# Kernel tuning notes

Hardware: AMD Instinct MI355X
Metric: run time of the kernel (lower is better)

## Reference

```python
import jax, jax.numpy as jnp
import numpy as np

EPS = 1e-5  # torch BatchNorm1d default eps


def _bn(h, scale, bias):
    # BatchNorm in training mode: biased variance over the node/edge dim.
    mu = h.mean(0)
    var = h.var(0)
    return (h - mu) * jax.lax.rsqrt(var + EPS) * scale + bias


def _segment_mean(msg, idx, n):
    s = jax.ops.segment_sum(msg, idx, num_segments=n)
    cnt = jax.ops.segment_sum(jnp.ones((msg.shape[0],), msg.dtype), idx, num_segments=n)
    return s / jnp.maximum(cnt, 1.0)[:, None]


def setup_inputs() -> dict:
    N, E, D, L = 50000, 800000, 64, 3
    key = jax.random.key(0)
    ks = jax.random.split(key, 7)
    return {
        "x": jax.random.normal(ks[0], (N, D), jnp.float32),
        "edge_attr": jax.random.normal(ks[1], (E, D), jnp.float32),
        "edge_index": jax.random.randint(ks[2], (2, E), 0, N, dtype=jnp.int32),
        "v_w": jax.random.normal(ks[3], (L, 4, D, D), jnp.float32) / np.sqrt(D),
        "v_b": jax.random.normal(ks[4], (L, 4, D), jnp.float32) * 0.02,
        "e_w": jax.random.normal(ks[5], (L, D, D), jnp.float32) / np.sqrt(D),
        "e_b": jax.random.normal(ks[6], (L, D), jnp.float32) * 0.02,
        "vbn_scale": jnp.ones((L, D), jnp.float32),
        "vbn_bias": jnp.zeros((L, D), jnp.float32),
        "ebn_scale": jnp.ones((L, D), jnp.float32),
        "ebn_bias": jnp.zeros((L, D), jnp.float32),
    }


def reference(x, edge_attr, edge_index, v_w, v_b, e_w, e_b,
              vbn_scale, vbn_bias, ebn_scale, ebn_bias):
    n = x.shape[0]
    dst = edge_index[0]  # aggregation target (scatter index)
    src = edge_index[1]  # neighbor node (gather index)
    num_layers = v_w.shape[0]
    w = edge_attr
    for l in range(num_layers):
        x0, w0 = x, w
        # Four node projections in one einsum: [4, N, D]
        xp = jnp.einsum('nd,kde->kne', x0, v_w[l]) + v_b[l][:, None, :]
        x1, x2, x3, x4 = xp[0], xp[1], xp[2], xp[3]
        # Anisotropic edge-gated message passing (vertex update)
        msg = jax.nn.sigmoid(w0) * x2[src]              # [E, D]
        agg = _segment_mean(msg, dst, n)                # [N, D]
        x = x0 + jax.nn.silu(_bn(x1 + agg, vbn_scale[l], vbn_bias[l]))
        # Edge update
        w1 = w0 @ e_w[l] + e_b[l]
        w = w0 + jax.nn.silu(_bn(w1 + x3[dst] + x4[src], ebn_scale[l], ebn_bias[l]))
    return x, w
```

## Files before the change

kernel.cpp:

```cpp
#include <hip/hip_runtime.h>
#include <hip/hip_bf16.h>
#include <math.h>

typedef __attribute__((ext_vector_type(8))) short bf16x8;
typedef __attribute__((ext_vector_type(4))) float f32x4;

__device__ __forceinline__ float bflo(unsigned u) { return __uint_as_float(u << 16); }
__device__ __forceinline__ float bfhi(unsigned u) { return __uint_as_float(u & 0xffff0000u); }
__device__ __forceinline__ unsigned packbf(float a, float b) {
    unsigned ua = __float_as_uint(a), ub = __float_as_uint(b);
    ua += 0x7fffu + ((ua >> 16) & 1u);
    ub += 0x7fffu + ((ub >> 16) & 1u);
    return (ua >> 16) | (ub & 0xffff0000u);
}
__device__ __forceinline__ float silu(float g) { return g / (1.f + __expf(-g)); }

__global__ void zero_int_kernel(int* __restrict__ p, int n) {
    int i = blockIdx.x * blockDim.x + threadIdx.x;
    int s = gridDim.x * blockDim.x;
    for (; i < n; i += s) p[i] = 0;
}

__global__ void count_kernel(const int* __restrict__ dst, int* __restrict__ cnt, int E) {
    int e = blockIdx.x * blockDim.x + threadIdx.x;
    if (e < E) atomicAdd(&cnt[dst[e]], 1);
}

__global__ __launch_bounds__(1024)
void scan_block_kernel(const int* __restrict__ cnt, int* __restrict__ off,
                       int* __restrict__ bsum, int n) {
    __shared__ int wsum[16];
    int tid = threadIdx.x, lane = tid & 63, wid = tid >> 6;
    int i = blockIdx.x * 1024 + tid;
    int v = (i < n) ? cnt[i] : 0;
    int sc = v;
    #pragma unroll
    for (int s = 1; s < 64; s <<= 1) {
        int t = __shfl_up(sc, (unsigned)s, 64);
        if (lane >= s) sc += t;
    }
    if (lane == 63) wsum[wid] = sc;
    __syncthreads();
    int woff = 0;
    for (int k = 0; k < wid; k++) woff += wsum[k];
    if (i < n) off[i + 1] = woff + sc;
    if (tid == 0) {
        int t = 0;
        #pragma unroll
        for (int k = 0; k < 16; k++) t += wsum[k];
        bsum[blockIdx.x] = t;
    }
}

__global__ void scan_tops_kernel(int* __restrict__ bsum, int nb) {
    int lane = threadIdx.x;
    int v = (lane < nb) ? bsum[lane] : 0;
    int sc = v;
    #pragma unroll
    for (int s = 1; s < 64; s <<= 1) {
        int t = __shfl_up(sc, (unsigned)s, 64);
        if (lane >= s) sc += t;
    }
    if (lane < nb) bsum[lane] = sc - v;
}

__global__ __launch_bounds__(1024)
void scan_add_kernel(int* __restrict__ off, const int* __restrict__ bsum, int n) {
    int i = blockIdx.x * 1024 + threadIdx.x;
    int b = bsum[blockIdx.x];
    if (i < n) off[i + 1] += b;
    if (i == 0) off[0] = 0;
}

__global__ void fill_csr_kernel(const int* __restrict__ dst, const int* __restrict__ src,
                                const int* __restrict__ off, int* __restrict__ cnt,
                                int* __restrict__ eidx, int* __restrict__ dstc,
                                int* __restrict__ srcc, int E) {
    int e = blockIdx.x * blockDim.x + threadIdx.x;
    if (e < E) {
        int d = dst[e];
        int pos = atomicSub(&cnt[d], 1) - 1;
        int slot = off[d] + pos;
        eidx[slot] = e;
        dstc[slot] = d;
        srcc[slot] = src[e];
    }
}

__global__ void pack_kernel(const float* __restrict__ v_w, const float* __restrict__ e_w,
                            short* __restrict__ vwp, short* __restrict__ ewp, int L) {
    int t = blockIdx.x * blockDim.x + threadIdx.x;
    if (t >= L * 5 * 4 * 2 * 64) return;
    int lane = t & 63;
    int ks = (t >> 6) & 1;
    int ft = (t >> 7) & 3;
    int mat = t >> 9;
    int layer = mat / 5, mi = mat % 5;
    const float* W = (mi < 4) ? (v_w + (long long)(layer * 4 + mi) * 4096)
                              : (e_w + (long long)layer * 4096);
    int m = ft * 16 + (lane & 15);
    int k0 = ks * 32 + (lane >> 4) * 8;
    short* dstp = (mi < 4)
        ? vwp + ((((long long)(layer * 4 + mi) * 4 + ft) * 2 + ks) * 64 + lane) * 8
        : ewp + ((((long long)layer * 4 + ft) * 2 + ks) * 64 + lane) * 8;
    #pragma unroll
    for (int j = 0; j < 8; j++) {
        unsigned u = __float_as_uint(W[(k0 + j) * 64 + m]);
        u += 0x7fffu + ((u >> 16) & 1u);
        dstp[j] = (short)(u >> 16);
    }
}

__global__ __launch_bounds__(256)
void node_gemm_mfma(const float* __restrict__ X, const short* __restrict__ vwp,
                    const float* __restrict__ vb, __hip_bfloat16* __restrict__ xp,
                    int Nn) {
    __shared__ short Xs[64 * 64];
    __shared__ short Hs[4][64 * 64];
    int tid = threadIdx.x;
    long long row0 = (long long)blockIdx.x * 64;

    {
        int r = tid >> 2, cq = tid & 3;
        long long row = row0 + r;
        float4 v0 = {0,0,0,0}, v1 = {0,0,0,0}, v2 = {0,0,0,0}, v3 = {0,0,0,0};
        if (row < Nn) {
            const float* sp = X + row * 64 + cq * 16;
            v0 = *(const float4*)(sp);     v1 = *(const float4*)(sp + 4);
            v2 = *(const float4*)(sp + 8); v3 = *(const float4*)(sp + 12);
        }
        uint4 w0, w1;
        w0.x = packbf(v0.x, v0.y); w0.y = packbf(v0.z, v0.w);
        w0.z = packbf(v1.x, v1.y); w0.w = packbf(v1.z, v1.w);
        w1.x = packbf(v2.x, v2.y); w1.y = packbf(v2.z, v2.w);
        w1.z = packbf(v3.x, v3.y); w1.w = packbf(v3.z, v3.w);
        int base = r * 128 + cq * 32, swz = (r & 7) << 4;
        *(uint4*)((char*)Xs + (base ^ swz)) = w0;
        *(uint4*)((char*)Xs + ((base + 16) ^ swz)) = w1;
    }
    __syncthreads();

    int l = tid & 63, wv = tid >> 6;
    int rl = wv * 16 + (l & 15);
    bf16x8 bfr[2];
    #pragma unroll
    for (int ks = 0; ks < 2; ks++) {
        int off = (rl * 128 + ks * 64 + (l >> 4) * 16) ^ ((rl & 7) << 4);
        bfr[ks] = *(bf16x8*)((char*)Xs + off);
    }
    int q4 = (l >> 4) * 4;
    for (int g = 0; g < 4; g++) {
        #pragma unroll
        for (int ft = 0; ft < 4; ft++) {
            f32x4 acc = f32x4{0.f, 0.f, 0.f, 0.f};
            #pragma unroll
            for (int ks = 0; ks < 2; ks++) {
                bf16x8 a = *(const bf16x8*)(vwp + (((long long)(g * 4 + ft) * 2 + ks) * 64 + l) * 8);
                acc = __builtin_amdgcn_mfma_f32_16x16x32_bf16(a, bfr[ks], acc, 0, 0, 0);
            }
            int f0 = ft * 16 + q4;
            float4 bv = *(const float4*)&vb[g * 64 + f0];
            uint2 o;
            o.x = packbf(acc[0] + bv.x, acc[1] + bv.y);
            o.y = packbf(acc[2] + bv.z, acc[3] + bv.w);
            int hoff = (rl * 128 + f0 * 2) ^ ((rl & 7) << 4);
            *(uint2*)((char*)Hs[g] + hoff) = o;
        }
    }
    __syncthreads();
    int r = tid >> 2, cc = (tid & 3) * 16;
    long long node = row0 + r;
    if (node < Nn) {
        int swz = (r & 7) << 4;
        #pragma unroll
        for (int g = 0; g < 4; g++) {
            uint4 a = *(uint4*)((char*)Hs[g] + ((r * 128 + cc * 2) ^ swz));
            uint4 b = *(uint4*)((char*)Hs[g] + ((r * 128 + cc * 2 + 16) ^ swz));
            __hip_bfloat16* op = xp + ((long long)g * Nn + node) * 64 + cc;
            *(uint4*)op = a;
            *(uint4*)(op + 8) = b;
        }
    }
}

template <int MODE>
__global__ __launch_bounds__(256)
void edge_gemm_mfma(const float* __restrict__ ea, const int* __restrict__ eidx,
                    __hip_bfloat16* __restrict__ w_csr, __hip_bfloat16* __restrict__ h_e,
                    const float* __restrict__ fin,
                    const short* __restrict__ ewp, const float* __restrict__ eb,
                    const __hip_bfloat16* __restrict__ x3, const __hip_bfloat16* __restrict__ x4,
                    const int* __restrict__ dstc, const int* __restrict__ srcc,
                    float* __restrict__ estats) {
    __shared__ short Ws[64 * 64];
    __shared__ short Hs[64 * 68];
    __shared__ float sredS[4][64], sredQ[4][64];
    __shared__ int dstl[64], srcl[64];
    int tid = threadIdx.x;
    long long row0 = (long long)blockIdx.x * 64;

    {
        int r = tid >> 2, cq = tid & 3;
        long long grow = (row0 + r) * 64 + cq * 16;
        int base = r * 128 + cq * 32, swz = (r & 7) << 4;
        uint4 w0u, w1u;
        if (MODE == 0) {
            long long e0 = eidx[row0 + r];
            const float* sp = ea + e0 * 64 + cq * 16;
            float4 v0 = *(const float4*)(sp),     v1 = *(const float4*)(sp + 4);
            float4 v2 = *(const float4*)(sp + 8), v3 = *(const float4*)(sp + 12);
            w0u.x = packbf(v0.x, v0.y); w0u.y = packbf(v0.z, v0.w);
            w0u.z = packbf(v1.x, v1.y); w0u.w = packbf(v1.z, v1.w);
            w1u.x = packbf(v2.x, v2.y); w1u.y = packbf(v2.z, v2.w);
            w1u.z = packbf(v3.x, v3.y); w1u.w = packbf(v3.z, v3.w);
        } else {
            uint4 a = *(const uint4*)&w_csr[grow];
            uint4 b = *(const uint4*)&w_csr[grow + 8];
            unsigned ua[8] = {a.x, a.y, a.z, a.w, b.x, b.y, b.z, b.w};
            uint4 ha = *(const uint4*)&h_e[grow];
            uint4 hb = *(const uint4*)&h_e[grow + 8];
            unsigned uh[8] = {ha.x, ha.y, ha.z, ha.w, hb.x, hb.y, hb.z, hb.w};
            const float* kmp = fin + 128 + cq * 16;
            const float* kap = fin + 192 + cq * 16;
            float wn[16];
            #pragma unroll
            for (int j = 0; j < 8; j++) {
                wn[2*j]   = bflo(ua[j]) + silu(bflo(uh[j]) * kmp[2*j]   + kap[2*j]);
                wn[2*j+1] = bfhi(ua[j]) + silu(bfhi(uh[j]) * kmp[2*j+1] + kap[2*j+1]);
            }
            w0u.x = packbf(wn[0], wn[1]);  w0u.y = packbf(wn[2], wn[3]);
            w0u.z = packbf(wn[4], wn[5]);  w0u.w = packbf(wn[6], wn[7]);
            w1u.x = packbf(wn[8], wn[9]);  w1u.y = packbf(wn[10], wn[11]);
            w1u.z = packbf(wn[12], wn[13]); w1u.w = packbf(wn[14], wn[15]);
        }
        *(uint4*)&w_csr[grow] = w0u;
        *(uint4*)&w_csr[grow + 8] = w1u;
        *(uint4*)((char*)Ws + (base ^ swz)) = w0u;
        *(uint4*)((char*)Ws + ((base + 16) ^ swz)) = w1u;
        if (tid < 64) {
            dstl[tid] = dstc[row0 + tid];
            srcl[tid] = srcc[row0 + tid];
        }
    }
    __syncthreads();

    int rr0 = tid >> 3, rr1 = rr0 + 32;
    int c8 = (tid & 7) * 8;
    int de0 = dstl[rr0], se0 = srcl[rr0];
    int de1 = dstl[rr1], se1 = srcl[rr1];
    uint4 g3a = *(const uint4*)&x3[(long long)de0 * 64 + c8];
    uint4 g4a = *(const uint4*)&x4[(long long)se0 * 64 + c8];
    uint4 g3b = *(const uint4*)&x3[(long long)de1 * 64 + c8];
    uint4 g4b = *(const uint4*)&x4[(long long)se1 * 64 + c8];

    int l = tid & 63, wv = tid >> 6;
    int rl = wv * 16 + (l & 15);
    bf16x8 bfr[2];
    #pragma unroll
    for (int ks = 0; ks < 2; ks++) {
        int off = (rl * 128 + ks * 64 + (l >> 4) * 16) ^ ((rl & 7) << 4);
        bfr[ks] = *(bf16x8*)((char*)Ws + off);
    }
    int q4 = (l >> 4) * 4;
    #pragma unroll
    for (int ft = 0; ft < 4; ft++) {
        f32x4 acc = f32x4{0.f, 0.f, 0.f, 0.f};
        #pragma unroll
        for (int ks = 0; ks < 2; ks++) {
            bf16x8 a = *(const bf16x8*)(ewp + (((long long)ft * 2 + ks) * 64 + l) * 8);
            acc = __builtin_amdgcn_mfma_f32_16x16x32_bf16(a, bfr[ks], acc, 0, 0, 0);
        }
        int f0 = ft * 16 + q4;
        float4 bv = *(const float4*)&eb[f0];
        uint2 o;
        o.x = packbf(acc[0] + bv.x, acc[1] + bv.y);
        o.y = packbf(acc[2] + bv.z, acc[3] + bv.w);
        *(uint2*)&Hs[rl * 68 + f0] = o;
    }
    __syncthreads();

    float s[8], q[8];
    #pragma unroll
    for (int j = 0; j < 8; j++) { s[j] = 0.f; q[j] = 0.f; }
    #pragma unroll
    for (int p = 0; p < 2; p++) {
        int rr = p ? rr1 : rr0;
        uint4 g3 = p ? g3b : g3a;
        uint4 g4 = p ? g4b : g4a;
        unsigned u3[4] = {g3.x, g3.y, g3.z, g3.w};
        unsigned u4[4] = {g4.x, g4.y, g4.z, g4.w};
        uint4 hu = *(uint4*)&Hs[rr * 68 + c8];
        unsigned uh[4] = {hu.x, hu.y, hu.z, hu.w};
        float h[8];
        #pragma unroll
        for (int j = 0; j < 4; j++) {
            float h0 = bflo(uh[j]) + bflo(u3[j]) + bflo(u4[j]);
            float h1 = bfhi(uh[j]) + bfhi(u3[j]) + bfhi(u4[j]);
            h[2*j] = h0; h[2*j+1] = h1;
            s[2*j] += h0; s[2*j+1] += h1;
            q[2*j] += h0 * h0; q[2*j+1] += h1 * h1;
        }
        uint4 hv;
        hv.x = packbf(h[0], h[1]); hv.y = packbf(h[2], h[3]);
        hv.z = packbf(h[4], h[5]); hv.w = packbf(h[6], h[7]);
        *(uint4*)&h_e[(row0 + rr) * 64 + c8] = hv;
    }
    #pragma unroll
    for (int d = 8; d < 64; d <<= 1) {
        #pragma unroll
        for (int j = 0; j < 8; j++) {
            s[j] += __shfl_xor(s[j], d);
            q[j] += __shfl_xor(q[j], d);
        }
    }
    if ((l >> 3) == 0) {
        #pragma unroll
        for (int j = 0; j < 8; j++) {
            sredS[wv][(l & 7) * 8 + j] = s[j];
            sredQ[wv][(l & 7) * 8 + j] = q[j];
        }
    }
    __syncthreads();
    if (tid < 128) {
        int which = tid >> 6, f = tid & 63;
        float v = which ? (sredQ[0][f] + sredQ[1][f] + sredQ[2][f] + sredQ[3][f])
                        : (sredS[0][f] + sredS[1][f] + sredS[2][f] + sredS[3][f]);
        atomicAdd(&estats[(blockIdx.x & 7) * 128 + which * 64 + f], v);
    }
}

template <bool FINAL>
__global__ __launch_bounds__(256)
void node_finish_kernel(const __hip_bfloat16* __restrict__ w_csr, const int* __restrict__ srcc,
                        const __hip_bfloat16* __restrict__ x2, const __hip_bfloat16* __restrict__ x1,
                        const int* __restrict__ off, float* __restrict__ h_v,
                        float* __restrict__ nstats,
                        const __hip_bfloat16* __restrict__ h_e, const int* __restrict__ eidx,
                        float* __restrict__ out_w, const float* __restrict__ fin,
                        int Nn, int E) {
    __shared__ float red[8 * 66];
    __shared__ float km[64], ka[64];
    int tid = threadIdx.x;
    if (FINAL) {
        if (tid < 64) { km[tid] = fin[128 + tid]; ka[tid] = fin[192 + tid]; }
        __syncthreads();
    }
    int hw = tid >> 5, k = tid & 31;
    int n = blockIdx.x * 8 + hw;
    float h0 = 0.f, h1 = 0.f;
    if (n < Nn) {
        int o0 = off[n], o1 = off[n + 1];
        float a0 = 0.f, a1 = 0.f;
        int j = o0;
        for (; j + 1 < o1; j += 2) {
            int s0 = srcc[j], s1 = srcc[j + 1];
            unsigned wu0 = *(const unsigned*)&w_csr[(long long)j * 64 + 2 * k];
            unsigned wu1 = *(const unsigned*)&w_csr[(long long)(j + 1) * 64 + 2 * k];
            unsigned xu0 = *(const unsigned*)&x2[(long long)s0 * 64 + 2 * k];
            unsigned xu1 = *(const unsigned*)&x2[(long long)s1 * 64 + 2 * k];
            a0 += bflo(xu0) / (1.f + __expf(-bflo(wu0)))
                + bflo(xu1) / (1.f + __expf(-bflo(wu1)));
            a1 += bfhi(xu0) / (1.f + __expf(-bfhi(wu0)))
                + bfhi(xu1) / (1.f + __expf(-bfhi(wu1)));
        }
        if (j < o1) {
            int s0 = srcc[j];
            unsigned wu0 = *(const unsigned*)&w_csr[(long long)j * 64 + 2 * k];
            unsigned xu0 = *(const unsigned*)&x2[(long long)s0 * 64 + 2 * k];
            a0 += bflo(xu0) / (1.f + __expf(-bflo(wu0)));
            a1 += bfhi(xu0) / (1.f + __expf(-bfhi(wu0)));
        }
        float ic = 1.f / fmaxf((float)(o1 - o0), 1.f);
        unsigned xu = *(const unsigned*)&x1[(long long)n * 64 + 2 * k];
        h0 = bflo(xu) + a0 * ic;
        h1 = bfhi(xu) + a1 * ic;
        *(float2*)&h_v[(long long)n * 64 + 2 * k] = make_float2(h0, h1);
    }
    red[hw * 66 + 2 * k] = h0;
    red[hw * 66 + 2 * k + 1] = h1;
    __syncthreads();
    float* nst = nstats + (blockIdx.x & 7) * 128;
    if (tid < 64) {
        float s = 0.f;
        #pragma unroll
        for (int r = 0; r < 8; r++) s += red[r * 66 + tid];
        atomicAdd(&nst[tid], s);
    }
    __syncthreads();
    red[hw * 66 + 2 * k] = h0 * h0;
    red[hw * 66 + 2 * k + 1] = h1 * h1;
    __syncthreads();
    if (tid < 64) {
        float s = 0.f;
        #pragma unroll
        for (int r = 0; r < 8; r++) s += red[r * 66 + tid];
        atomicAdd(&nst[64 + tid], s);
    }
    if (FINAL) {
        long long total = (long long)E * 32;
        for (long long u = (long long)blockIdx.x * 256 + tid; u < total;
             u += (long long)gridDim.x * 256) {
            long long row = u >> 5;
            int kk = (int)(u & 31);
            unsigned wu = *(const unsigned*)&w_csr[row * 64 + 2 * kk];
            unsigned hu = *(const unsigned*)&h_e[row * 64 + 2 * kk];
            int e = eidx[row];
            float o0 = bflo(wu) + silu(bflo(hu) * km[2 * kk]     + ka[2 * kk]);
            float o1 = bfhi(wu) + silu(bfhi(hu) * km[2 * kk + 1] + ka[2 * kk + 1]);
            *(float2*)&out_w[(long long)e * 64 + 2 * kk] = make_float2(o0, o1);
        }
    }
}

__global__ void finalize_edge_kernel(const float* __restrict__ estats,
                                     const float* __restrict__ es, const float* __restrict__ eb,
                                     float* __restrict__ fin, float invE) {
    int c = threadIdx.x;
    float s = 0.f, q = 0.f;
    #pragma unroll
    for (int r = 0; r < 8; r++) { s += estats[r * 128 + c]; q += estats[r * 128 + 64 + c]; }
    float mean = s * invE;
    float var = q * invE - mean * mean;
    float kmul = rsqrtf(var + 1e-5f) * es[c];
    fin[128 + c] = kmul;
    fin[192 + c] = eb[c] - mean * kmul;
}

__global__ void finalize_node_kernel(const float* __restrict__ nstats,
                                     const float* __restrict__ vs, const float* __restrict__ vb,
                                     float* __restrict__ fin, float invN) {
    int c = threadIdx.x;
    float s = 0.f, q = 0.f;
    #pragma unroll
    for (int r = 0; r < 8; r++) { s += nstats[r * 128 + c]; q += nstats[r * 128 + 64 + c]; }
    float mean = s * invN;
    float var = q * invN - mean * mean;
    float kmul = rsqrtf(var + 1e-5f) * vs[c];
    fin[c] = kmul;
    fin[64 + c] = vb[c] - mean * kmul;
}

__global__ __launch_bounds__(256)
void node_apply_kernel(const float4* __restrict__ hv4, const float4* __restrict__ xold4,
                       float4* __restrict__ out4, const float* __restrict__ fin, int total) {
    __shared__ float km[64], ka[64];
    if (threadIdx.x < 64) { km[threadIdx.x] = fin[threadIdx.x]; ka[threadIdx.x] = fin[64 + threadIdx.x]; }
    __syncthreads();
    int idx = blockIdx.x * 256 + threadIdx.x;
    if (idx >= total) return;
    int c0 = (idx & 15) * 4;
    float4 h = hv4[idx], xo = xold4[idx];
    float4 m = *(float4*)&km[c0], a = *(float4*)&ka[c0];
    float g0 = h.x * m.x + a.x, g1 = h.y * m.y + a.y, g2 = h.z * m.z + a.z, g3 = h.w * m.w + a.w;
    out4[idx] = make_float4(xo.x + silu(g0), xo.y + silu(g1),
                            xo.z + silu(g2), xo.w + silu(g3));
}

extern "C" void kernel_launch(void* const* d_in, const int* in_sizes, int n_in,
                              void* d_out, int out_size, void* d_ws, size_t ws_size,
                              hipStream_t stream) {
    const float* x_in  = (const float*)d_in[0];
    const float* ea_in = (const float*)d_in[1];
    const int*   ei    = (const int*)d_in[2];
    const float* v_w   = (const float*)d_in[3];
    const float* v_b   = (const float*)d_in[4];
    const float* e_w   = (const float*)d_in[5];
    const float* e_b   = (const float*)d_in[6];
    const float* vbn_s = (const float*)d_in[7];
    const float* vbn_b = (const float*)d_in[8];
    const float* ebn_s = (const float*)d_in[9];
    const float* ebn_b = (const float*)d_in[10];

    const int Nn = in_sizes[0] / 64;
    const int E  = in_sizes[1] / 64;
    const int L  = in_sizes[3] / (4 * 64 * 64);

    const int* dst = ei;
    const int* src = ei + E;

    float* h_v    = (float*)d_ws;
    float* nstats = h_v + (long long)Nn * 64;
    float* estats = nstats + (long long)L * 1024;
    float* fin    = estats + (long long)L * 1024;
    __hip_bfloat16* xp    = (__hip_bfloat16*)(fin + 256);
    __hip_bfloat16* h_e   = xp + (long long)4 * Nn * 64;
    __hip_bfloat16* w_csr = h_e + (long long)E * 64;
    short* vwp = (short*)(w_csr + (long long)E * 64);
    short* ewp = vwp + (long long)L * 16384;
    int* cnt  = (int*)(ewp + (long long)L * 4096);
    int* off  = cnt + Nn;
    int* eidx = off + Nn + 1;
    int* dstc = eidx + E;
    int* srcc = dstc + E;
    int* bsum = srcc + E;

    size_t needed = ((size_t)Nn * 64 + (size_t)L * 2048 + 256) * 4 +
                    ((size_t)4 * Nn * 64 + (size_t)2 * E * 64 + (size_t)L * 20480) * 2 +
                    ((size_t)2 * Nn + 1 + (size_t)3 * E + 64) * 4;
    if (ws_size < needed) return;

    float* out_x = (float*)d_out;
    float* out_w = out_x + (long long)Nn * 64;

    const int nb = (Nn + 1023) / 1024;
    zero_int_kernel<<<64, 256, 0, stream>>>(cnt, Nn);
    zero_int_kernel<<<8, 256, 0, stream>>>((int*)nstats, L * 2048);
    count_kernel<<<(E + 255) / 256, 256, 0, stream>>>(dst, cnt, E);
    scan_block_kernel<<<nb, 1024, 0, stream>>>(cnt, off, bsum, Nn);
    scan_tops_kernel<<<1, 64, 0, stream>>>(bsum, nb);
    scan_add_kernel<<<nb, 1024, 0, stream>>>(off, bsum, Nn);
    fill_csr_kernel<<<(E + 255) / 256, 256, 0, stream>>>(dst, src, off, cnt, eidx, dstc, srcc, E);
    pack_kernel<<<(L * 2560 + 255) / 256, 256, 0, stream>>>(v_w, e_w, vwp, ewp, L);

    const __hip_bfloat16* x1 = xp;
    const __hip_bfloat16* x2 = xp + (long long)Nn * 64;
    const __hip_bfloat16* x3 = xp + (long long)2 * Nn * 64;
    const __hip_bfloat16* x4 = xp + (long long)3 * Nn * 64;

    for (int l = 0; l < L; l++) {
        const float* xl = (l == 0) ? x_in : out_x;
        bool last = (l == L - 1);
        float* nst = nstats + (long long)l * 1024;
        float* est = estats + (long long)l * 1024;

        node_gemm_mfma<<<(Nn + 63) / 64, 256, 0, stream>>>(
            xl, vwp + (long long)l * 16384, v_b + l * 256, xp, Nn);

        if (l == 0)
            edge_gemm_mfma<0><<<E / 64, 256, 0, stream>>>(
                ea_in, eidx, w_csr, h_e, fin, ewp + (long long)l * 4096, e_b + l * 64,
                x3, x4, dstc, srcc, est);
        else
            edge_gemm_mfma<1><<<E / 64, 256, 0, stream>>>(
                ea_in, eidx, w_csr, h_e, fin, ewp + (long long)l * 4096, e_b + l * 64,
                x3, x4, dstc, srcc, est);

        finalize_edge_kernel<<<1, 64, 0, stream>>>(
            est, ebn_s + l * 64, ebn_b + l * 64, fin, 1.f / (float)E);

        if (last)
            node_finish_kernel<true><<<(Nn + 7) / 8, 256, 0, stream>>>(
                w_csr, srcc, x2, x1, off, h_v, nst, h_e, eidx, out_w, fin, Nn, E);
        else
            node_finish_kernel<false><<<(Nn + 7) / 8, 256, 0, stream>>>(
                w_csr, srcc, x2, x1, off, h_v, nst, h_e, eidx, out_w, fin, Nn, E);

        finalize_node_kernel<<<1, 64, 0, stream>>>(
            nst, vbn_s + l * 64, vbn_b + l * 64, fin, 1.f / (float)Nn);

        node_apply_kernel<<<(Nn * 16 + 255) / 256, 256, 0, stream>>>(
            (const float4*)h_v, (const float4*)xl, (float4*)out_x, fin, Nn * 16);
    }
}
```

Before: 718.0 us.

## Recompute previous-layer edge pre-activation instead of storing h_e; fuse final edge output

Intermediate layers no longer write the bf16 edge pre-activation h_e. The next layer's edge kernel instead recomputes it from the previous layer's weights and double-buffered x3/x4 projections, then applies the BN/SiLU residual update in shared memory. The final edge output write moves into the node_finish CSR loop rather than running as a separate grid-stride pass. This trades E*64 bf16 of store plus reload traffic per layer for an extra small MFMA GEMM and extra gathers, and it doubles the node projection buffer.

```diff
diff --git a/kernel.cpp b/kernel.cpp
--- a/kernel.cpp
+++ b/kernel.cpp
@@ -183,12 +183,14 @@
     }
 }
 
-template <int MODE>
+template <bool FIRST, bool LAST>
 __global__ __launch_bounds__(256)
 void edge_gemm_mfma(const float* __restrict__ ea, const int* __restrict__ eidx,
                     __hip_bfloat16* __restrict__ w_csr, __hip_bfloat16* __restrict__ h_e,
                     const float* __restrict__ fin,
+                    const short* __restrict__ ewp_p, const float* __restrict__ eb_p,
                     const short* __restrict__ ewp, const float* __restrict__ eb,
+                    const __hip_bfloat16* __restrict__ x3p, const __hip_bfloat16* __restrict__ x4p,
                     const __hip_bfloat16* __restrict__ x3, const __hip_bfloat16* __restrict__ x4,
                     const int* __restrict__ dstc, const int* __restrict__ srcc,
                     float* __restrict__ estats) {
@@ -204,7 +206,7 @@
         long long grow = (row0 + r) * 64 + cq * 16;
         int base = r * 128 + cq * 32, swz = (r & 7) << 4;
         uint4 w0u, w1u;
-        if (MODE == 0) {
+        if (FIRST) {
             long long e0 = eidx[row0 + r];
             const float* sp = ea + e0 * 64 + cq * 16;
             float4 v0 = *(const float4*)(sp),     v1 = *(const float4*)(sp + 4);
@@ -213,28 +215,12 @@
             w0u.z = packbf(v1.x, v1.y); w0u.w = packbf(v1.z, v1.w);
             w1u.x = packbf(v2.x, v2.y); w1u.y = packbf(v2.z, v2.w);
             w1u.z = packbf(v3.x, v3.y); w1u.w = packbf(v3.z, v3.w);
+            *(uint4*)&w_csr[grow] = w0u;
+            *(uint4*)&w_csr[grow + 8] = w1u;
         } else {
-            uint4 a = *(const uint4*)&w_csr[grow];
-            uint4 b = *(const uint4*)&w_csr[grow + 8];
-            unsigned ua[8] = {a.x, a.y, a.z, a.w, b.x, b.y, b.z, b.w};
-            uint4 ha = *(const uint4*)&h_e[grow];
-            uint4 hb = *(const uint4*)&h_e[grow + 8];
-            unsigned uh[8] = {ha.x, ha.y, ha.z, ha.w, hb.x, hb.y, hb.z, hb.w};
-            const float* kmp = fin + 128 + cq * 16;
-            const float* kap = fin + 192 + cq * 16;
-            float wn[16];
-            #pragma unroll
-            for (int j = 0; j < 8; j++) {
-                wn[2*j]   = bflo(ua[j]) + silu(bflo(uh[j]) * kmp[2*j]   + kap[2*j]);
-                wn[2*j+1] = bfhi(ua[j]) + silu(bfhi(uh[j]) * kmp[2*j+1] + kap[2*j+1]);
-            }
-            w0u.x = packbf(wn[0], wn[1]);  w0u.y = packbf(wn[2], wn[3]);
-            w0u.z = packbf(wn[4], wn[5]);  w0u.w = packbf(wn[6], wn[7]);
-            w1u.x = packbf(wn[8], wn[9]);  w1u.y = packbf(wn[10], wn[11]);
-            w1u.z = packbf(wn[12], wn[13]); w1u.w = packbf(wn[14], wn[15]);
-        }
-        *(uint4*)&w_csr[grow] = w0u;
-        *(uint4*)&w_csr[grow + 8] = w1u;
+            w0u = *(const uint4*)&w_csr[grow];
+            w1u = *(const uint4*)&w_csr[grow + 8];
+        }
         *(uint4*)((char*)Ws + (base ^ swz)) = w0u;
         *(uint4*)((char*)Ws + ((base + 16) ^ swz)) = w1u;
         if (tid < 64) {
@@ -244,24 +230,86 @@
     }
     __syncthreads();
 
+    int l = tid & 63, wv = tid >> 6;
+    int rl = wv * 16 + (l & 15);
+    int q4 = (l >> 4) * 4;
     int rr0 = tid >> 3, rr1 = rr0 + 32;
     int c8 = (tid & 7) * 8;
     int de0 = dstl[rr0], se0 = srcl[rr0];
     int de1 = dstl[rr1], se1 = srcl[rr1];
+
+    if (!FIRST) {
+        uint4 p3a = *(const uint4*)&x3p[(long long)de0 * 64 + c8];
+        uint4 p4a = *(const uint4*)&x4p[(long long)se0 * 64 + c8];
+        uint4 p3b = *(const uint4*)&x3p[(long long)de1 * 64 + c8];
+        uint4 p4b = *(const uint4*)&x4p[(long long)se1 * 64 + c8];
+
+        bf16x8 bfr[2];
+        #pragma unroll
+        for (int ks = 0; ks < 2; ks++) {
+            int off = (rl * 128 + ks * 64 + (l >> 4) * 16) ^ ((rl & 7) << 4);
+            bfr[ks] = *(bf16x8*)((char*)Ws + off);
+        }
+        #pragma unroll
+        for (int ft = 0; ft < 4; ft++) {
+            f32x4 acc = f32x4{0.f, 0.f, 0.f, 0.f};
+            #pragma unroll
+            for (int ks = 0; ks < 2; ks++) {
+                bf16x8 a = *(const bf16x8*)(ewp_p + (((long long)ft * 2 + ks) * 64 + l) * 8);
+                acc = __builtin_amdgcn_mfma_f32_16x16x32_bf16(a, bfr[ks], acc, 0, 0, 0);
+            }
+            int f0 = ft * 16 + q4;
+            float4 bv = *(const float4*)&eb_p[f0];
+            uint2 o;
+            o.x = packbf(acc[0] + bv.x, acc[1] + bv.y);
+            o.y = packbf(acc[2] + bv.z, acc[3] + bv.w);
+            *(uint2*)&Hs[rl * 68 + f0] = o;
+        }
+        __syncthreads();
+
+        float4 km0 = *(const float4*)&fin[128 + c8], km1 = *(const float4*)&fin[128 + c8 + 4];
+        float4 ka0 = *(const float4*)&fin[192 + c8], ka1 = *(const float4*)&fin[192 + c8 + 4];
+        float kmv[8] = {km0.x, km0.y, km0.z, km0.w, km1.x, km1.y, km1.z, km1.w};
+        float kav[8] = {ka0.x, ka0.y, ka0.z, ka0.w, ka1.x, ka1.y, ka1.z, ka1.w};
+        #pragma unroll
+        for (int p = 0; p < 2; p++) {
+            int rr = p ? rr1 : rr0;
+            uint4 p3 = p ? p3b : p3a;
+            uint4 p4 = p ? p4b : p4a;
+            unsigned u3[4] = {p3.x, p3.y, p3.z, p3.w};
+            unsigned u4[4] = {p4.x, p4.y, p4.z, p4.w};
+            uint4 hu = *(uint4*)&Hs[rr * 68 + c8];
+            unsigned uh[4] = {hu.x, hu.y, hu.z, hu.w};
+            int woff = (rr * 128 + c8 * 2) ^ ((rr & 7) << 4);
+            uint4 wu = *(uint4*)((char*)Ws + woff);
+            unsigned uw[4] = {wu.x, wu.y, wu.z, wu.w};
+            float wn[8];
+            #pragma unroll
+            for (int j = 0; j < 4; j++) {
+                float h0 = bflo(uh[j]) + bflo(u3[j]) + bflo(u4[j]);
+                float h1 = bfhi(uh[j]) + bfhi(u3[j]) + bfhi(u4[j]);
+                wn[2*j]   = bflo(uw[j]) + silu(h0 * kmv[2*j]   + kav[2*j]);
+                wn[2*j+1] = bfhi(uw[j]) + silu(h1 * kmv[2*j+1] + kav[2*j+1]);
+            }
+            uint4 wo;
+            wo.x = packbf(wn[0], wn[1]); wo.y = packbf(wn[2], wn[3]);
+            wo.z = packbf(wn[4], wn[5]); wo.w = packbf(wn[6], wn[7]);
+            *(uint4*)((char*)Ws + woff) = wo;
+            *(uint4*)&w_csr[(row0 + rr) * 64 + c8] = wo;
+        }
+        __syncthreads();
+    }
+
     uint4 g3a = *(const uint4*)&x3[(long long)de0 * 64 + c8];
     uint4 g4a = *(const uint4*)&x4[(long long)se0 * 64 + c8];
     uint4 g3b = *(const uint4*)&x3[(long long)de1 * 64 + c8];
     uint4 g4b = *(const uint4*)&x4[(long long)se1 * 64 + c8];
-
-    int l = tid & 63, wv = tid >> 6;
-    int rl = wv * 16 + (l & 15);
     bf16x8 bfr[2];
     #pragma unroll
     for (int ks = 0; ks < 2; ks++) {
         int off = (rl * 128 + ks * 64 + (l >> 4) * 16) ^ ((rl & 7) << 4);
         bfr[ks] = *(bf16x8*)((char*)Ws + off);
     }
-    int q4 = (l >> 4) * 4;
     #pragma unroll
     for (int ft = 0; ft < 4; ft++) {
         f32x4 acc = f32x4{0.f, 0.f, 0.f, 0.f};
@@ -300,10 +348,12 @@
             s[2*j] += h0; s[2*j+1] += h1;
             q[2*j] += h0 * h0; q[2*j+1] += h1 * h1;
         }
-        uint4 hv;
-        hv.x = packbf(h[0], h[1]); hv.y = packbf(h[2], h[3]);
-        hv.z = packbf(h[4], h[5]); hv.w = packbf(h[6], h[7]);
-        *(uint4*)&h_e[(row0 + rr) * 64 + c8] = hv;
+        if (LAST) {
+            uint4 hv;
+            hv.x = packbf(h[0], h[1]); hv.y = packbf(h[2], h[3]);
+            hv.z = packbf(h[4], h[5]); hv.w = packbf(h[6], h[7]);
+            *(uint4*)&h_e[(row0 + rr) * 64 + c8] = hv;
+        }
     }
     #pragma unroll
     for (int d = 8; d < 64; d <<= 1) {
@@ -336,8 +386,7 @@
                         const int* __restrict__ off, float* __restrict__ h_v,
                         float* __restrict__ nstats,
                         const __hip_bfloat16* __restrict__ h_e, const int* __restrict__ eidx,
-                        float* __restrict__ out_w, const float* __restrict__ fin,
-                        int Nn, int E) {
+                        float* __restrict__ out_w, const float* __restrict__ fin, int Nn) {
     __shared__ float red[8 * 66];
     __shared__ float km[64], ka[64];
     int tid = threadIdx.x;
@@ -362,6 +411,17 @@
                 + bflo(xu1) / (1.f + __expf(-bflo(wu1)));
             a1 += bfhi(xu0) / (1.f + __expf(-bfhi(wu0)))
                 + bfhi(xu1) / (1.f + __expf(-bfhi(wu1)));
+            if (FINAL) {
+                unsigned hu0 = *(const unsigned*)&h_e[(long long)j * 64 + 2 * k];
+                unsigned hu1 = *(const unsigned*)&h_e[(long long)(j + 1) * 64 + 2 * k];
+                int e0 = eidx[j], e1 = eidx[j + 1];
+                float o00 = bflo(wu0) + silu(bflo(hu0) * km[2*k]   + ka[2*k]);
+                float o01 = bfhi(wu0) + silu(bfhi(hu0) * km[2*k+1] + ka[2*k+1]);
+                float o10 = bflo(wu1) + silu(bflo(hu1) * km[2*k]   + ka[2*k]);
+                float o11 = bfhi(wu1) + silu(bfhi(hu1) * km[2*k+1] + ka[2*k+1]);
+                *(float2*)&out_w[(long long)e0 * 64 + 2 * k] = make_float2(o00, o01);
+                *(float2*)&out_w[(long long)e1 * 64 + 2 * k] = make_float2(o10, o11);
+            }
         }
         if (j < o1) {
             int s0 = srcc[j];
@@ -369,6 +429,13 @@
             unsigned xu0 = *(const unsigned*)&x2[(long long)s0 * 64 + 2 * k];
             a0 += bflo(xu0) / (1.f + __expf(-bflo(wu0)));
             a1 += bfhi(xu0) / (1.f + __expf(-bfhi(wu0)));
+            if (FINAL) {
+                unsigned hu0 = *(const unsigned*)&h_e[(long long)j * 64 + 2 * k];
+                int e0 = eidx[j];
+                float o00 = bflo(wu0) + silu(bflo(hu0) * km[2*k]   + ka[2*k]);
+                float o01 = bfhi(wu0) + silu(bfhi(hu0) * km[2*k+1] + ka[2*k+1]);
+                *(float2*)&out_w[(long long)e0 * 64 + 2 * k] = make_float2(o00, o01);
+            }
         }
         float ic = 1.f / fmaxf((float)(o1 - o0), 1.f);
         unsigned xu = *(const unsigned*)&x1[(long long)n * 64 + 2 * k];
@@ -395,20 +462,6 @@
         #pragma unroll
         for (int r = 0; r < 8; r++) s += red[r * 66 + tid];
         atomicAdd(&nst[64 + tid], s);
-    }
-    if (FINAL) {
-        long long total = (long long)E * 32;
-        for (long long u = (long long)blockIdx.x * 256 + tid; u < total;
-             u += (long long)gridDim.x * 256) {
-            long long row = u >> 5;
-            int kk = (int)(u & 31);
-            unsigned wu = *(const unsigned*)&w_csr[row * 64 + 2 * kk];
-            unsigned hu = *(const unsigned*)&h_e[row * 64 + 2 * kk];
-            int e = eidx[row];
-            float o0 = bflo(wu) + silu(bflo(hu) * km[2 * kk]     + ka[2 * kk]);
-            float o1 = bfhi(wu) + silu(bfhi(hu) * km[2 * kk + 1] + ka[2 * kk + 1]);
-            *(float2*)&out_w[(long long)e * 64 + 2 * kk] = make_float2(o0, o1);
-        }
     }
 }
 
@@ -482,8 +535,9 @@
     float* nstats = h_v + (long long)Nn * 64;
     float* estats = nstats + (long long)L * 1024;
     float* fin    = estats + (long long)L * 1024;
-    __hip_bfloat16* xp    = (__hip_bfloat16*)(fin + 256);
-    __hip_bfloat16* h_e   = xp + (long long)4 * Nn * 64;
+    __hip_bfloat16* xp0   = (__hip_bfloat16*)(fin + 256);
+    __hip_bfloat16* xp1   = xp0 + (long long)4 * Nn * 64;
+    __hip_bfloat16* h_e   = xp1 + (long long)4 * Nn * 64;
     __hip_bfloat16* w_csr = h_e + (long long)E * 64;
     short* vwp = (short*)(w_csr + (long long)E * 64);
     short* ewp = vwp + (long long)L * 16384;
@@ -495,7 +549,7 @@
     int* bsum = srcc + E;
 
     size_t needed = ((size_t)Nn * 64 + (size_t)L * 2048 + 256) * 4 +
-                    ((size_t)4 * Nn * 64 + (size_t)2 * E * 64 + (size_t)L * 20480) * 2 +
+                    ((size_t)8 * Nn * 64 + (size_t)2 * E * 64 + (size_t)L * 20480) * 2 +
                     ((size_t)2 * Nn + 1 + (size_t)3 * E + 64) * 4;
     if (ws_size < needed) return;
 
@@ -512,38 +566,54 @@
     fill_csr_kernel<<<(E + 255) / 256, 256, 0, stream>>>(dst, src, off, cnt, eidx, dstc, srcc, E);
     pack_kernel<<<(L * 2560 + 255) / 256, 256, 0, stream>>>(v_w, e_w, vwp, ewp, L);
 
-    const __hip_bfloat16* x1 = xp;
-    const __hip_bfloat16* x2 = xp + (long long)Nn * 64;
-    const __hip_bfloat16* x3 = xp + (long long)2 * Nn * 64;
-    const __hip_bfloat16* x4 = xp + (long long)3 * Nn * 64;
-
     for (int l = 0; l < L; l++) {
         const float* xl = (l == 0) ? x_in : out_x;
+        bool first = (l == 0);
         bool last = (l == L - 1);
         float* nst = nstats + (long long)l * 1024;
         float* est = estats + (long long)l * 1024;
+        __hip_bfloat16* xp_cur  = (l & 1) ? xp1 : xp0;
+        __hip_bfloat16* xp_prev = (l & 1) ? xp0 : xp1;
+        const __hip_bfloat16* x1 = xp_cur;
+        const __hip_bfloat16* x2 = xp_cur + (long long)Nn * 64;
+        const __hip_bfloat16* x3 = xp_cur + (long long)2 * Nn * 64;
+        const __hip_bfloat16* x4 = xp_cur + (long long)3 * Nn * 64;
+        const __hip_bfloat16* x3p = xp_prev + (long long)2 * Nn * 64;
+        const __hip_bfloat16* x4p = xp_prev + (long long)3 * Nn * 64;
 
         node_gemm_mfma<<<(Nn + 63) / 64, 256, 0, stream>>>(
-            xl, vwp + (long long)l * 16384, v_b + l * 256, xp, Nn);
-
-        if (l == 0)
-            edge_gemm_mfma<0><<<E / 64, 256, 0, stream>>>(
-                ea_in, eidx, w_csr, h_e, fin, ewp + (long long)l * 4096, e_b + l * 64,
-                x3, x4, dstc, srcc, est);
+            xl, vwp + (long long)l * 16384, v_b + l * 256, xp_cur, Nn);
+
+        const short* ewp_c = ewp + (long long)l * 4096;
+        const short* ewp_pv = (l > 0) ? ewp + (long long)(l - 1) * 4096 : ewp_c;
+        const float* eb_c = e_b + l * 64;
+        const float* eb_pv = (l > 0) ? e_b + (l - 1) * 64 : eb_c;
+        if (first && !last)
+            edge_gemm_mfma<true, false><<<E / 64, 256, 0, stream>>>(
+                ea_in, eidx, w_csr, h_e, fin, ewp_pv, eb_pv, ewp_c, eb_c,
+                x3p, x4p, x3, x4, dstc, srcc, est);
+        else if (first && last)
+            edge_gemm_mfma<true, true><<<E / 64, 256, 0, stream>>>(
+                ea_in, eidx, w_csr, h_e, fin, ewp_pv, eb_pv, ewp_c, eb_c,
+                x3p, x4p, x3, x4, dstc, srcc, est);
+        else if (!first && !last)
+            edge_gemm_mfma<false, false><<<E / 64, 256, 0, stream>>>(
+                ea_in, eidx, w_csr, h_e, fin, ewp_pv, eb_pv, ewp_c, eb_c,
+                x3p, x4p, x3, x4, dstc, srcc, est);
         else
-            edge_gemm_mfma<1><<<E / 64, 256, 0, stream>>>(
-                ea_in, eidx, w_csr, h_e, fin, ewp + (long long)l * 4096, e_b + l * 64,
-                x3, x4, dstc, srcc, est);
+            edge_gemm_mfma<false, true><<<E / 64, 256, 0, stream>>>(
+                ea_in, eidx, w_csr, h_e, fin, ewp_pv, eb_pv, ewp_c, eb_c,
+                x3p, x4p, x3, x4, dstc, srcc, est);
 
         finalize_edge_kernel<<<1, 64, 0, stream>>>(
             est, ebn_s + l * 64, ebn_b + l * 64, fin, 1.f / (float)E);
 
         if (last)
             node_finish_kernel<true><<<(Nn + 7) / 8, 256, 0, stream>>>(
-                w_csr, srcc, x2, x1, off, h_v, nst, h_e, eidx, out_w, fin, Nn, E);
+                w_csr, srcc, x2, x1, off, h_v, nst, h_e, eidx, out_w, fin, Nn);
         else
             node_finish_kernel<false><<<(Nn + 7) / 8, 256, 0, stream>>>(
-                w_csr, srcc, x2, x1, off, h_v, nst, h_e, eidx, out_w, fin, Nn, E);
+                w_csr, srcc, x2, x1, off, h_v, nst, h_e, eidx, out_w, fin, Nn);
 
         finalize_node_kernel<<<1, 64, 0, stream>>>(
             nst, vbn_s + l * 64, vbn_b + l * 64, fin, 1.f / (float)Nn);
```

Result: faster. 698.1 us (-2.8%).
